# Kernel optimization log

Hardware: AMD Instinct MI355X
Metric: run time of the kernel (lower is better)

## Reference

```python
import jax, jax.numpy as jnp
import numpy as np


def lstm_scan(x, W, U, b, hidden):
    """Keras-style LSTM. x: [B,T,D]. Returns full hidden sequence [B,T,H].
    Gate order i,f,c,o; sigmoid recurrent activation, tanh cell activation."""
    B, T, D = x.shape
    H = hidden
    # Precompute input projections for all timesteps in one big GEMM: [B,T,4H]
    xz = jnp.einsum('btd,dk->btk', x, W) + b
    xz = jnp.transpose(xz, (1, 0, 2))  # [T,B,4H] for scan

    def step(carry, xz_t):
        h, c = carry
        z = xz_t + h @ U  # [B,4H]
        i = jax.nn.sigmoid(z[:, 0*H:1*H])
        f = jax.nn.sigmoid(z[:, 1*H:2*H])
        g = jnp.tanh(z[:, 2*H:3*H])
        o = jax.nn.sigmoid(z[:, 3*H:4*H])
        c_new = f * c + i * g
        h_new = o * jnp.tanh(c_new)
        return (h_new, c_new), h_new

    h0 = jnp.zeros((B, H), dtype=x.dtype)
    c0 = jnp.zeros((B, H), dtype=x.dtype)
    _, hs = jax.lax.scan(step, (h0, c0), xz)  # hs: [T,B,H]
    return jnp.transpose(hs, (1, 0, 2))  # [B,T,H]


def setup_inputs() -> dict:
    key = jax.random.key(0)
    ks = jax.random.split(key, 9)
    B, T, D = 512, 512, 300
    H1, H2, C = 128, 32, 14
    s = lambda fan: 1.0 / np.sqrt(fan)
    return {
        'x':  jax.random.normal(ks[0], (B, T, D), dtype=jnp.float32),
        'W1': jax.random.normal(ks[1], (D, 4 * H1), dtype=jnp.float32) * s(D),
        'U1': jax.random.normal(ks[2], (H1, 4 * H1), dtype=jnp.float32) * s(H1),
        'b1': jnp.zeros((4 * H1,), dtype=jnp.float32),
        'W2': jax.random.normal(ks[3], (H1, 4 * H2), dtype=jnp.float32) * s(H1),
        'U2': jax.random.normal(ks[4], (H2, 4 * H2), dtype=jnp.float32) * s(H2),
        'b2': jnp.zeros((4 * H2,), dtype=jnp.float32),
        'Wd': jax.random.normal(ks[5], (H2, C), dtype=jnp.float32) * s(H2),
        'bd': jnp.zeros((C,), dtype=jnp.float32),
    }


def reference(x, W1, U1, b1, W2, U2, b2, Wd, bd):
    h1 = lstm_scan(x, W1, U1, b1, 128)      # [B,T,128] (return_sequences=True)
    h2 = lstm_scan(h1, W2, U2, b2, 32)      # [B,T,32]
    h2_last = h2[:, -1, :]                  # return_sequences=False -> last step
    return jax.nn.softmax(h2_last @ Wd + bd, axis=-1)  # [B,14]
```

## Files before the change

kernel.cpp:

```cpp
#include <hip/hip_runtime.h>
#include <math.h>

#define TC 128
#define NC 4
#define BATCH 512
#define T_TOTAL 512
#define D_IN 300
#define KP1 320
#define H1 128
#define G1 512
#define H2 32
#define NCLS 14

typedef unsigned short u16;
typedef __attribute__((ext_vector_type(8))) _Float16 f16x8;
typedef __attribute__((ext_vector_type(4))) float f32x4;

__device__ __forceinline__ float fexp2(float x) { return __builtin_amdgcn_exp2f(x); }
__device__ __forceinline__ float frcp(float x)  { return __builtin_amdgcn_rcpf(x); }
__device__ __forceinline__ float sig_f(float x) { return frcp(1.0f + fexp2(-1.44269504f * x)); }
__device__ __forceinline__ float th_f(float x)  { return 1.0f - 2.0f * frcp(1.0f + fexp2(2.88539008f * x)); }

__device__ __forceinline__ void lds_barrier() {
    asm volatile("s_waitcnt lgkmcnt(0)" ::: "memory");
    __builtin_amdgcn_s_barrier();
}

__global__ void prep_weights(const float* __restrict__ U1, _Float16* __restrict__ U1p,
                             const float* __restrict__ U2, _Float16* __restrict__ U2p,
                             const float* __restrict__ W1, _Float16* __restrict__ W1T,
                             const float* __restrict__ W2, _Float16* __restrict__ W2T,
                             const float* __restrict__ b1, float* __restrict__ b1p,
                             const float* __restrict__ b2, float* __restrict__ b2p)
{
    int idx = blockIdx.x * 256 + threadIdx.x;
    if (idx < 512 * 128) {
        int p = idx >> 7, k = idx & 127;
        int orig = ((p >> 4) & 3) * 128 + ((p >> 6) << 4) + (p & 15);
        U1p[p * 128 + k] = (_Float16)U1[k * 512 + orig];
    }
    if (idx < 512 * 320) {
        int p = idx / 320, k = idx % 320;
        int orig = ((p >> 4) & 3) * 128 + ((p >> 6) << 4) + (p & 15);
        W1T[p * 320 + k] = (_Float16)((k < D_IN) ? W1[k * 512 + orig] : 0.f);
    }
    if (idx < 128 * 128) {
        int p = idx >> 7, k = idx & 127;
        int orig = ((p >> 4) & 3) * 32 + ((p >> 6) << 4) + (p & 15);
        W2T[p * 128 + k] = (_Float16)W2[k * 128 + orig];
    }
    if (idx < 128 * 32) {
        int p = idx >> 5, k = idx & 31;
        int orig = ((p >> 4) & 3) * 32 + ((p >> 6) << 4) + (p & 15);
        U2p[p * 32 + k] = (_Float16)U2[k * 128 + orig];
    }
    if (idx < 512) {
        int orig = ((idx >> 4) & 3) * 128 + ((idx >> 6) << 4) + (idx & 15);
        b1p[idx] = b1[orig];
    }
    if (idx < 128) {
        int orig = ((idx >> 4) & 3) * 32 + ((idx >> 6) << 4) + (idx & 15);
        b2p[idx] = b2[orig];
    }
}

__device__ __forceinline__ void xsplit_item(const float* __restrict__ x,
                                            _Float16* __restrict__ xh,
                                            int chunk, long i)
{
    int rr = (int)(i / 40), s = (int)(i % 40);
    int b = rr >> 7, tt = rr & 127;
    long m = (long)b * T_TOTAL + (long)chunk * TC + tt;
    int k0 = s * 8;
    const float* xr = x + m * D_IN + k0;
    float4 v0 = {0.f, 0.f, 0.f, 0.f}, v1 = {0.f, 0.f, 0.f, 0.f};
    if (s < 37) {
        v0 = *(const float4*)(xr);
        v1 = *(const float4*)(xr + 4);
    } else if (s == 37) {
        v0 = *(const float4*)(xr);
    }
    f16x8 o;
    o[0] = (_Float16)v0.x; o[1] = (_Float16)v0.y;
    o[2] = (_Float16)v0.z; o[3] = (_Float16)v0.w;
    o[4] = (_Float16)v1.x; o[5] = (_Float16)v1.y;
    o[6] = (_Float16)v1.z; o[7] = (_Float16)v1.w;
    *(f16x8*)(xh + m * KP1 + k0) = o;
}

__global__ void xsplit_chunk(const float* __restrict__ x, _Float16* __restrict__ xh, int chunk)
{
    long gid = (long)blockIdx.x * 256 + threadIdx.x;
    if (gid >= 65536L * 40) return;
    xsplit_item(x, xh, chunk, gid);
}

__device__ __forceinline__ void xsplit_role(const float* __restrict__ x,
                                            _Float16* __restrict__ xh,
                                            int chunk, int cwid, int ncw)
{
    const int tid = threadIdx.x;
    for (long i = (long)cwid * 512 + tid; i < 65536L * 40; i += (long)ncw * 512)
        xsplit_item(x, xh, chunk, i);
}

template<int NK, int NT, bool XMAP>
__device__ __forceinline__ void gemm_mblock(
    const _Float16* __restrict__ A, const _Float16* __restrict__ B,
    const float* __restrict__ bias, float* __restrict__ C,
    int m0, int chunk)
{
    const int Nc = NT * 128;
    const int tid = threadIdx.x;
    const int l = tid & 63, w = tid >> 6;
    const int wm = w >> 2, wn = w & 3;
    const int lr = l & 15, q = l >> 4;
    const int koff = q * 8;
    const int LDA = NK * 32;

    const _Float16* ap[4];
#pragma unroll
    for (int fi = 0; fi < 4; fi++) {
        int m = m0 + wm * 64 + fi * 16 + lr;
        long row = XMAP ? ((long)(m >> 7) * T_TOTAL + (long)chunk * TC + (m & (TC - 1)))
                        : (long)m;
        ap[fi] = A + row * LDA + koff;
    }
    const _Float16* bp[NT * 2];
    float bv[NT * 2];
#pragma unroll
    for (int fj = 0; fj < NT * 2; fj++) {
        int col = (fj >> 1) * 128 + wn * 32 + (fj & 1) * 16 + lr;
        bp[fj] = B + (long)col * LDA + koff;
        bv[fj] = bias[col];
    }

    f32x4 acc[4][NT * 2];
#pragma unroll
    for (int fi = 0; fi < 4; fi++)
#pragma unroll
        for (int fj = 0; fj < NT * 2; fj++)
            acc[fi][fj] = (f32x4){bv[fj], bv[fj], bv[fj], bv[fj]};

    f16x8 acur[4], anxt[4];
#pragma unroll
    for (int fi = 0; fi < 4; fi++)
        acur[fi] = *(const f16x8*)(ap[fi]);

#pragma unroll
    for (int ks = 0; ks < NK; ks++) {
        f16x8 bb[NT * 2];
#pragma unroll
        for (int fj = 0; fj < NT * 2; fj++)
            bb[fj] = *(const f16x8*)(bp[fj] + ks * 32);
        if (ks + 1 < NK) {
#pragma unroll
            for (int fi = 0; fi < 4; fi++)
                anxt[fi] = *(const f16x8*)(ap[fi] + (ks + 1) * 32);
        }
#pragma unroll
        for (int fi = 0; fi < 4; fi++)
#pragma unroll
            for (int fj = 0; fj < NT * 2; fj++)
                acc[fi][fj] = __builtin_amdgcn_mfma_f32_16x16x32_f16(acur[fi], bb[fj], acc[fi][fj], 0, 0, 0);
#pragma unroll
        for (int fi = 0; fi < 4; fi++)
            acur[fi] = anxt[fi];
    }

#pragma unroll
    for (int fi = 0; fi < 4; fi++) {
        int mrow = m0 + wm * 64 + fi * 16 + q * 4;
#pragma unroll
        for (int fj = 0; fj < NT * 2; fj++) {
            int col = (fj >> 1) * 128 + wn * 32 + (fj & 1) * 16 + lr;
#pragma unroll
            for (int rr = 0; rr < 4; rr++)
                C[(long)(mrow + rr) * Nc + col] = acc[fi][fj][rr];
        }
    }
}

#define L1_DECL(P) float P##0, P##1, P##2, P##3, P##4, P##5, P##6, P##7;

#define L1_LOAD(P, T)                                                             \
    P##0 = xz[xrA + (long)(T) * 512 +  0]; P##1 = xz[xrB + (long)(T) * 512 +  0]; \
    P##2 = xz[xrA + (long)(T) * 512 + 16]; P##3 = xz[xrB + (long)(T) * 512 + 16]; \
    P##4 = xz[xrA + (long)(T) * 512 + 32]; P##5 = xz[xrB + (long)(T) * 512 + 32]; \
    P##6 = xz[xrA + (long)(T) * 512 + 48]; P##7 = xz[xrB + (long)(T) * 512 + 48];

#define L1_STEP(T, PB, XC, XN)                                                    \
{                                                                                 \
    f16x8 ah0 = *(const f16x8*)&Ah[(PB) * 2048 + lr * 128 + (((q     ) ^ lr) << 3)]; \
    f16x8 ah1 = *(const f16x8*)&Ah[(PB) * 2048 + lr * 128 + (((q +  4) ^ lr) << 3)]; \
    f16x8 ah2 = *(const f16x8*)&Ah[(PB) * 2048 + lr * 128 + (((q +  8) ^ lr) << 3)]; \
    f16x8 ah3 = *(const f16x8*)&Ah[(PB) * 2048 + lr * 128 + (((q + 12) ^ lr) << 3)]; \
    if ((T) + 1 < TC) { L1_LOAD(XN, (T) + 1) }                                    \
    f32x4 a0 = (f32x4){XC##0, XC##1, 0.f, 0.f};                                   \
    f32x4 a1 = (f32x4){XC##2, XC##3, 0.f, 0.f};                                   \
    f32x4 a2 = (f32x4){XC##4, XC##5, 0.f, 0.f};                                   \
    f32x4 a3 = (f32x4){XC##6, XC##7, 0.f, 0.f};                                   \
    a0 = __builtin_amdgcn_mfma_f32_16x16x32_f16(ah0, uh00, a0, 0, 0, 0);          \
    a1 = __builtin_amdgcn_mfma_f32_16x16x32_f16(ah0, uh10, a1, 0, 0, 0);          \
    a2 = __builtin_amdgcn_mfma_f32_16x16x32_f16(ah0, uh20, a2, 0, 0, 0);          \
    a3 = __builtin_amdgcn_mfma_f32_16x16x32_f16(ah0, uh30, a3, 0, 0, 0);          \
    a0 = __builtin_amdgcn_mfma_f32_16x16x32_f16(ah1, uh01, a0, 0, 0, 0);          \
    a1 = __builtin_amdgcn_mfma_f32_16x16x32_f16(ah1, uh11, a1, 0, 0, 0);          \
    a2 = __builtin_amdgcn_mfma_f32_16x16x32_f16(ah1, uh21, a2, 0, 0, 0);          \
    a3 = __builtin_amdgcn_mfma_f32_16x16x32_f16(ah1, uh31, a3, 0, 0, 0);          \
    a0 = __builtin_amdgcn_mfma_f32_16x16x32_f16(ah2, uh02, a0, 0, 0, 0);          \
    a1 = __builtin_amdgcn_mfma_f32_16x16x32_f16(ah2, uh12, a1, 0, 0, 0);          \
    a2 = __builtin_amdgcn_mfma_f32_16x16x32_f16(ah2, uh22, a2, 0, 0, 0);          \
    a3 = __builtin_amdgcn_mfma_f32_16x16x32_f16(ah2, uh32, a3, 0, 0, 0);          \
    a0 = __builtin_amdgcn_mfma_f32_16x16x32_f16(ah3, uh03, a0, 0, 0, 0);          \
    a1 = __builtin_amdgcn_mfma_f32_16x16x32_f16(ah3, uh13, a1, 0, 0, 0);          \
    a2 = __builtin_amdgcn_mfma_f32_16x16x32_f16(ah3, uh23, a2, 0, 0, 0);          \
    a3 = __builtin_amdgcn_mfma_f32_16x16x32_f16(ah3, uh33, a3, 0, 0, 0);          \
    {                                                                             \
        float iv = sig_f(a0[0]), fv = sig_f(a1[0]), gv = th_f(a2[0]), ov = sig_f(a3[0]); \
        cstA = fv * cstA + iv * gv;                                               \
        float hv = ov * th_f(cstA);                                               \
        _Float16 hh = (_Float16)hv;                                               \
        Ah[((PB) ^ 1) * 2048 + pA * 128 + idxA] = hh;                             \
        h1f[((long)(b0 + rA) * TC + (T)) * 128 + cn] = hh;                        \
        if ((T) == TC - 1) {                                                      \
            s1h[(long)(b0 + rA) * 128 + cn] = hv;                                 \
            s1c[(long)(b0 + rA) * 128 + cn] = cstA;                               \
        }                                                                         \
    }                                                                             \
    {                                                                             \
        float iv = sig_f(a0[1]), fv = sig_f(a1[1]), gv = th_f(a2[1]), ov = sig_f(a3[1]); \
        cstB = fv * cstB + iv * gv;                                               \
        float hv = ov * th_f(cstB);                                               \
        _Float16 hh = (_Float16)hv;                                               \
        Ah[((PB) ^ 1) * 2048 + pB * 128 + idxB] = hh;                             \
        h1f[((long)(b0 + rB) * TC + (T)) * 128 + cn] = hh;                        \
        if ((T) == TC - 1) {                                                      \
            s1h[(long)(b0 + rB) * 128 + cn] = hv;                                 \
            s1c[(long)(b0 + rB) * 128 + cn] = cstB;                               \
        }                                                                         \
    }                                                                             \
    lds_barrier();                                                                \
}

static __device__ __forceinline__ void lstm1_role(
    const float* __restrict__ xz, const _Float16* __restrict__ U1p,
    _Float16* __restrict__ h1f, float* __restrict__ s1h, float* __restrict__ s1c,
    int first, char* smc)
{
    const int tid = threadIdx.x;
    const int l = tid & 63, w = tid >> 6;
    const int lr = l & 15, q = l >> 4;
    const int koff = q * 8;
    const int cn = w * 16 + lr;
    const int b0 = blockIdx.x * 8;
    const int p0 = w * 64 + lr;
    const int rA = 2 * q, rB = 2 * q + 1;
    const int pA = 4 * q, pB = 4 * q + 1;
    const int idxA = (((cn >> 3) ^ pA) << 3) + (cn & 7);
    const int idxB = (((cn >> 3) ^ pB) << 3) + (cn & 7);

    _Float16* Ah = (_Float16*)smc;

    const long xrA = ((long)(b0 + rA) * TC) * 512 + p0;
    const long xrB = ((long)(b0 + rB) * TC) * 512 + p0;

    const _Float16* ub = U1p + (long)(w * 64 + lr) * 128 + koff;
    f16x8 uh00 = *(const f16x8*)(ub +    0 * 128 +  0);
    f16x8 uh01 = *(const f16x8*)(ub +    0 * 128 + 32);
    f16x8 uh02 = *(const f16x8*)(ub +    0 * 128 + 64);
    f16x8 uh03 = *(const f16x8*)(ub +    0 * 128 + 96);
    f16x8 uh10 = *(const f16x8*)(ub +   16 * 128 +  0);
    f16x8 uh11 = *(const f16x8*)(ub +   16 * 128 + 32);
    f16x8 uh12 = *(const f16x8*)(ub +   16 * 128 + 64);
    f16x8 uh13 = *(const f16x8*)(ub +   16 * 128 + 96);
    f16x8 uh20 = *(const f16x8*)(ub +   32 * 128 +  0);
    f16x8 uh21 = *(const f16x8*)(ub +   32 * 128 + 32);
    f16x8 uh22 = *(const f16x8*)(ub +   32 * 128 + 64);
    f16x8 uh23 = *(const f16x8*)(ub +   32 * 128 + 96);
    f16x8 uh30 = *(const f16x8*)(ub +   48 * 128 +  0);
    f16x8 uh31 = *(const f16x8*)(ub +   48 * 128 + 32);
    f16x8 uh32 = *(const f16x8*)(ub +   48 * 128 + 64);
    f16x8 uh33 = *(const f16x8*)(ub +   48 * 128 + 96);

    float hA = 0.f, hB = 0.f, cstA = 0.f, cstB = 0.f;
    if (!first) {
        hA = s1h[(long)(b0 + rA) * 128 + cn];
        cstA = s1c[(long)(b0 + rA) * 128 + cn];
        hB = s1h[(long)(b0 + rB) * 128 + cn];
        cstB = s1c[(long)(b0 + rB) * 128 + cn];
    }
    Ah[pA * 128 + idxA] = (_Float16)hA;
    Ah[pB * 128 + idxB] = (_Float16)hB;
    {
        int p2 = 4 * q + 2, p3 = 4 * q + 3;
        int idx2 = (((cn >> 3) ^ p2) << 3) + (cn & 7);
        int idx3 = (((cn >> 3) ^ p3) << 3) + (cn & 7);
        Ah[p2 * 128 + idx2] = (_Float16)0.f;
        Ah[p3 * 128 + idx3] = (_Float16)0.f;
        Ah[2048 + p2 * 128 + idx2] = (_Float16)0.f;
        Ah[2048 + p3 * 128 + idx3] = (_Float16)0.f;
    }
    lds_barrier();

    L1_DECL(xa) L1_DECL(xb)
    L1_LOAD(xa, 0)

    for (int t = 0; t < TC; t += 2) {
        L1_STEP(t,     0, xa, xb)
        L1_STEP(t + 1, 1, xb, xa)
    }
}

#define L2_DECL(P) float P##00, P##01, P##02, P##03, P##10, P##11, P##12, P##13, \
                         P##20, P##21, P##22, P##23, P##30, P##31, P##32, P##33;

#define L2_LOAD(P, T)                                                             \
    P##00 = xz2[yr0 + (long)(T) * 128 +  0]; P##01 = xz2[yr1 + (long)(T) * 128 +  0]; \
    P##02 = xz2[yr2 + (long)(T) * 128 +  0]; P##03 = xz2[yr3 + (long)(T) * 128 +  0]; \
    P##10 = xz2[yr0 + (long)(T) * 128 + 16]; P##11 = xz2[yr1 + (long)(T) * 128 + 16]; \
    P##12 = xz2[yr2 + (long)(T) * 128 + 16]; P##13 = xz2[yr3 + (long)(T) * 128 + 16]; \
    P##20 = xz2[yr0 + (long)(T) * 128 + 32]; P##21 = xz2[yr1 + (long)(T) * 128 + 32]; \
    P##22 = xz2[yr2 + (long)(T) * 128 + 32]; P##23 = xz2[yr3 + (long)(T) * 128 + 32]; \
    P##30 = xz2[yr0 + (long)(T) * 128 + 48]; P##31 = xz2[yr1 + (long)(T) * 128 + 48]; \
    P##32 = xz2[yr2 + (long)(T) * 128 + 48]; P##33 = xz2[yr3 + (long)(T) * 128 + 48];

#define L2_STEP(T, PB, XC, XN)                                                    \
{                                                                                 \
    if (act) {                                                                    \
        f16x8 ah = *(const f16x8*)&Ah[(PB) * 640 + lr * 40 + koff];               \
        if ((T) + 1 < TC) { L2_LOAD(XN, (T) + 1) }                                \
        f32x4 a0 = (f32x4){XC##00, XC##01, XC##02, XC##03};                       \
        f32x4 a1 = (f32x4){XC##10, XC##11, XC##12, XC##13};                       \
        f32x4 a2 = (f32x4){XC##20, XC##21, XC##22, XC##23};                       \
        f32x4 a3 = (f32x4){XC##30, XC##31, XC##32, XC##33};                       \
        a0 = __builtin_amdgcn_mfma_f32_16x16x32_f16(ah, uh0, a0, 0, 0, 0);        \
        a1 = __builtin_amdgcn_mfma_f32_16x16x32_f16(ah, uh1, a1, 0, 0, 0);        \
        a2 = __builtin_amdgcn_mfma_f32_16x16x32_f16(ah, uh2, a2, 0, 0, 0);        \
        a3 = __builtin_amdgcn_mfma_f32_16x16x32_f16(ah, uh3, a3, 0, 0, 0);        \
        _Pragma("unroll")                                                         \
        for (int r = 0; r < 4; r++) {                                             \
            float iv = sig_f(a0[r]);                                              \
            float fv = sig_f(a1[r]);                                              \
            float gv = th_f(a2[r]);                                               \
            float ov = sig_f(a3[r]);                                              \
            float cc = (r == 0) ? cst0 : (r == 1) ? cst1 : (r == 2) ? cst2 : cst3;\
            cc = fv * cc + iv * gv;                                               \
            float hv = ov * th_f(cc);                                             \
            if (r == 0) cst0 = cc; else if (r == 1) cst1 = cc;                    \
            else if (r == 2) cst2 = cc; else cst3 = cc;                           \
            int rw = (q << 2) + r;                                                \
            Ah[((PB) ^ 1) * 640 + rw * 40 + cn] = (_Float16)hv;                   \
            if ((T) == TC - 1) {                                                  \
                s2h[(long)(b0 + rw) * 32 + cn] = hv;                              \
                s2c[(long)(b0 + rw) * 32 + cn] = cc;                              \
            }                                                                     \
        }                                                                         \
    }                                                                             \
    lds_barrier();                                                                \
}

static __device__ __forceinline__ void lstm2_role(
    const float* __restrict__ xz2, const _Float16* __restrict__ U2p,
    float* __restrict__ s2h, float* __restrict__ s2c, int first, char* smc)
{
    const int tid = threadIdx.x;
    const int b0 = (blockIdx.x - 64) * 16;
    const bool act = tid < 128;
    const int l = tid & 63, w = (tid >> 6) & 1;
    const int lr = l & 15, q = l >> 4;
    const int koff = q * 8;
    const int cn = w * 16 + lr;
    const int p0 = w * 64 + lr;
    const int bq = b0 + q * 4;

    const long yr0 = ((long)(bq + 0) * TC) * 128 + p0;
    const long yr1 = ((long)(bq + 1) * TC) * 128 + p0;
    const long yr2 = ((long)(bq + 2) * TC) * 128 + p0;
    const long yr3 = ((long)(bq + 3) * TC) * 128 + p0;

    _Float16* Ah = (_Float16*)smc;

    f16x8 uh0 = {}, uh1 = {}, uh2 = {}, uh3 = {};
    float cst0 = 0.f, cst1 = 0.f, cst2 = 0.f, cst3 = 0.f;
    L2_DECL(xa) L2_DECL(xb)

    if (act) {
        const _Float16* ub = U2p + (long)(w * 64 + lr) * 32 + koff;
        uh0 = *(const f16x8*)(ub +  0 * 32);
        uh1 = *(const f16x8*)(ub + 16 * 32);
        uh2 = *(const f16x8*)(ub + 32 * 32);
        uh3 = *(const f16x8*)(ub + 48 * 32);
#pragma unroll
        for (int r = 0; r < 4; r++) {
            int rw = q * 4 + r;
            float h = 0.f, c = 0.f;
            if (!first) {
                h = s2h[(long)(b0 + rw) * 32 + cn];
                c = s2c[(long)(b0 + rw) * 32 + cn];
            }
            if (r == 0) cst0 = c; else if (r == 1) cst1 = c;
            else if (r == 2) cst2 = c; else cst3 = c;
            Ah[rw * 40 + cn] = (_Float16)h;
        }
        L2_LOAD(xa, 0)
    }
    lds_barrier();

    for (int t = 0; t < TC; t += 2) {
        L2_STEP(t,     0, xa, xb)
        L2_STEP(t + 1, 1, xb, xa)
    }
}

__global__ void
__attribute__((amdgpu_flat_work_group_size(512, 512)))
__attribute__((amdgpu_waves_per_eu(2, 2)))
mega(
    const float* __restrict__ x, _Float16* __restrict__ xh,
    const _Float16* __restrict__ W1T, const float* __restrict__ b1p,
    const _Float16* __restrict__ W2T, const float* __restrict__ b2p,
    const _Float16* __restrict__ U1p, const _Float16* __restrict__ U2p,
    float* xz1_0, float* xz1_1, float* xz2_0, float* xz2_1,
    _Float16* h1f_0, _Float16* h1f_1,
    float* s1h, float* s1c, float* s2h, float* s2c,
    int cA, int cB, int g1, int g2, int xs)
{
    __shared__ __align__(16) char sm[8192];
    int bid = blockIdx.x;

    if (cA >= 0 && bid < 64) {
        const float* xz = (cA & 1) ? xz1_1 : xz1_0;
        _Float16* hf = (cA & 1) ? h1f_1 : h1f_0;
        lstm1_role(xz, U1p, hf, s1h, s1c, cA == 0, sm);
        return;
    }
    if (cB >= 0 && bid >= 64 && bid < 96) {
        const float* xz2 = (cB & 1) ? xz2_1 : xz2_0;
        lstm2_role(xz2, U2p, s2h, s2c, cB == 0, sm);
        return;
    }
    int cwid = bid, ncw = 256;
    if (cA >= 0) { ncw -= 64; cwid -= 64; }
    if (cB >= 0) { ncw -= 32; if (bid >= 96) cwid -= 32; }
    if (xs >= 0) xsplit_role(x, xh, xs, cwid, ncw);
    int ng1 = (g1 >= 0) ? (BATCH * TC / 128) : 0;
    int ng2 = (g2 >= 0) ? (BATCH * TC / 128) : 0;
    float* xz1o = (g1 >= 0 && (g1 & 1)) ? xz1_1 : xz1_0;
    float* xz2o = (g2 >= 0 && (g2 & 1)) ? xz2_1 : xz2_0;
    const _Float16* hf = (g2 >= 0 && (g2 & 1)) ? h1f_1 : h1f_0;
    for (int it = cwid; it < ng1 + ng2; it += ncw) {
        if (it < ng1)
            gemm_mblock<10, 4, true>(xh, W1T, b1p, xz1o, it * 128, g1);
        else
            gemm_mblock<4, 1, false>(hf, W2T, b2p, xz2o, (it - ng1) * 128, 0);
    }
}

__global__ __launch_bounds__(256)
void head_kernel(const float* __restrict__ h2, const float* __restrict__ Wd,
                 const float* __restrict__ bd, float* __restrict__ out)
{
    int b = blockIdx.x * 256 + threadIdx.x;
    float h[H2];
#pragma unroll
    for (int k = 0; k < H2; k += 4)
        *(float4*)&h[k] = *(const float4*)&h2[b * H2 + k];

    float lg[NCLS];
#pragma unroll
    for (int c = 0; c < NCLS; c++) lg[c] = bd[c];
#pragma unroll
    for (int k = 0; k < H2; k++) {
        float hv = h[k];
#pragma unroll
        for (int c = 0; c < NCLS; c++)
            lg[c] += hv * Wd[k * NCLS + c];
    }
    float m = lg[0];
#pragma unroll
    for (int c = 1; c < NCLS; c++) m = fmaxf(m, lg[c]);
    float s = 0.f;
#pragma unroll
    for (int c = 0; c < NCLS; c++) { lg[c] = __expf(lg[c] - m); s += lg[c]; }
    float inv = __fdividef(1.0f, s);
#pragma unroll
    for (int c = 0; c < NCLS; c++) out[b * NCLS + c] = lg[c] * inv;
}

extern "C" void kernel_launch(void* const* d_in, const int* in_sizes, int n_in,
                              void* d_out, int out_size, void* d_ws, size_t ws_size,
                              hipStream_t stream)
{
    const float* x  = (const float*)d_in[0];
    const float* W1 = (const float*)d_in[1];
    const float* U1 = (const float*)d_in[2];
    const float* b1 = (const float*)d_in[3];
    const float* W2 = (const float*)d_in[4];
    const float* U2 = (const float*)d_in[5];
    const float* b2 = (const float*)d_in[6];
    const float* Wd = (const float*)d_in[7];
    const float* bd = (const float*)d_in[8];
    float* out = (float*)d_out;

    char* ws = (char*)d_ws;
    float* xz1[2]    = {(float*)(ws + 0L),         (float*)(ws + 134217728L)};
    _Float16* xh     = (_Float16*)(ws + 268435456L);
    _Float16* h1f[2] = {(_Float16*)(ws + 436207616L), (_Float16*)(ws + 452984832L)};
    float* xz2[2]    = {(float*)(ws + 469762048L), (float*)(ws + 503316480L)};
    float* s1h       = (float*)(ws + 536870912L);
    float* s1c       = (float*)(ws + 537133056L);
    float* s2h       = (float*)(ws + 537395200L);
    float* s2c       = (float*)(ws + 537460736L);
    _Float16* U1p    = (_Float16*)(ws + 537526272L);
    _Float16* U2p    = (_Float16*)(ws + 537657344L);
    _Float16* W1T    = (_Float16*)(ws + 537665536L);
    _Float16* W2T    = (_Float16*)(ws + 537993216L);
    float* b1p       = (float*)(ws + 538025984L);
    float* b2p       = (float*)(ws + 538028032L);

    prep_weights<<<640, 256, 0, stream>>>(U1, U1p, U2, U2p, W1, W1T, W2, W2T,
                                          b1, b1p, b2, b2p);
    xsplit_chunk<<<10240, 256, 0, stream>>>(x, xh, 0);

#define MEGA(cA_, cB_, g1_, g2_, xs_) \
    mega<<<256, 512, 0, stream>>>(x, xh, W1T, b1p, W2T, b2p, U1p, U2p, \
        xz1[0], xz1[1], xz2[0], xz2[1], h1f[0], h1f[1], \
        s1h, s1c, s2h, s2c, cA_, cB_, g1_, g2_, xs_)

    MEGA(-1, -1, 0, -1, 1);
    MEGA(0, -1, 1, -1, 2);
    MEGA(1, -1, 2, 0, 3);
    MEGA(2, 0, 3, 1, -1);
    MEGA(3, 1, -1, 2, -1);
    MEGA(-1, 2, -1, 3, -1);
    MEGA(-1, 3, -1, -1, -1);
#undef MEGA

    head_kernel<<<2, 256, 0, stream>>>(s2h, Wd, bd, out);
}
```

Before: 917.1 us.

## Split LSTM1 recurrence across 128 blocks with 4 batch rows each

The layer-1 recurrent role now handles 4 batch rows per workgroup instead of 8, so each lane processes one row and 128 blocks share the recurrence. To make room, the persistent mega kernel launches 512 blocks and raises waves_per_eu to 4, and the GEMM/xsplit worker indexing is recomputed to skip the LSTM blocks. The aim is to shorten the serial per-step critical path and raise occupancy. In exchange, half of each MFMA's accumulator rows do no useful work, the U1 fragments are loaded by twice as many blocks, and the tighter register budget may cause spills.

```diff
diff --git a/kernel.cpp b/kernel.cpp
--- a/kernel.cpp
+++ b/kernel.cpp
@@ -181,13 +181,13 @@
     }
 }
 
-#define L1_DECL(P) float P##0, P##1, P##2, P##3, P##4, P##5, P##6, P##7;
+#define L1_DECL(P) float P##0, P##1, P##2, P##3;
 
 #define L1_LOAD(P, T)                                                             \
-    P##0 = xz[xrA + (long)(T) * 512 +  0]; P##1 = xz[xrB + (long)(T) * 512 +  0]; \
-    P##2 = xz[xrA + (long)(T) * 512 + 16]; P##3 = xz[xrB + (long)(T) * 512 + 16]; \
-    P##4 = xz[xrA + (long)(T) * 512 + 32]; P##5 = xz[xrB + (long)(T) * 512 + 32]; \
-    P##6 = xz[xrA + (long)(T) * 512 + 48]; P##7 = xz[xrB + (long)(T) * 512 + 48];
+    P##0 = xz[xr + (long)(T) * 512 +  0];                                         \
+    P##1 = xz[xr + (long)(T) * 512 + 16];                                         \
+    P##2 = xz[xr + (long)(T) * 512 + 32];                                         \
+    P##3 = xz[xr + (long)(T) * 512 + 48];
 
 #define L1_STEP(T, PB, XC, XN)                                                    \
 {                                                                                 \
@@ -196,10 +196,10 @@
     f16x8 ah2 = *(const f16x8*)&Ah[(PB) * 2048 + lr * 128 + (((q +  8) ^ lr) << 3)]; \
     f16x8 ah3 = *(const f16x8*)&Ah[(PB) * 2048 + lr * 128 + (((q + 12) ^ lr) << 3)]; \
     if ((T) + 1 < TC) { L1_LOAD(XN, (T) + 1) }                                    \
-    f32x4 a0 = (f32x4){XC##0, XC##1, 0.f, 0.f};                                   \
-    f32x4 a1 = (f32x4){XC##2, XC##3, 0.f, 0.f};                                   \
-    f32x4 a2 = (f32x4){XC##4, XC##5, 0.f, 0.f};                                   \
-    f32x4 a3 = (f32x4){XC##6, XC##7, 0.f, 0.f};                                   \
+    f32x4 a0 = (f32x4){XC##0, 0.f, 0.f, 0.f};                                     \
+    f32x4 a1 = (f32x4){XC##1, 0.f, 0.f, 0.f};                                     \
+    f32x4 a2 = (f32x4){XC##2, 0.f, 0.f, 0.f};                                     \
+    f32x4 a3 = (f32x4){XC##3, 0.f, 0.f, 0.f};                                     \
     a0 = __builtin_amdgcn_mfma_f32_16x16x32_f16(ah0, uh00, a0, 0, 0, 0);          \
     a1 = __builtin_amdgcn_mfma_f32_16x16x32_f16(ah0, uh10, a1, 0, 0, 0);          \
     a2 = __builtin_amdgcn_mfma_f32_16x16x32_f16(ah0, uh20, a2, 0, 0, 0);          \
@@ -218,26 +218,14 @@
     a3 = __builtin_amdgcn_mfma_f32_16x16x32_f16(ah3, uh33, a3, 0, 0, 0);          \
     {                                                                             \
         float iv = sig_f(a0[0]), fv = sig_f(a1[0]), gv = th_f(a2[0]), ov = sig_f(a3[0]); \
-        cstA = fv * cstA + iv * gv;                                               \
-        float hv = ov * th_f(cstA);                                               \
+        cst = fv * cst + iv * gv;                                                 \
+        float hv = ov * th_f(cst);                                                \
         _Float16 hh = (_Float16)hv;                                               \
-        Ah[((PB) ^ 1) * 2048 + pA * 128 + idxA] = hh;                             \
-        h1f[((long)(b0 + rA) * TC + (T)) * 128 + cn] = hh;                        \
+        Ah[((PB) ^ 1) * 2048 + pq * 128 + idxq] = hh;                             \
+        h1f[((long)(b0 + q) * TC + (T)) * 128 + cn] = hh;                         \
         if ((T) == TC - 1) {                                                      \
-            s1h[(long)(b0 + rA) * 128 + cn] = hv;                                 \
-            s1c[(long)(b0 + rA) * 128 + cn] = cstA;                               \
-        }                                                                         \
-    }                                                                             \
-    {                                                                             \
-        float iv = sig_f(a0[1]), fv = sig_f(a1[1]), gv = th_f(a2[1]), ov = sig_f(a3[1]); \
-        cstB = fv * cstB + iv * gv;                                               \
-        float hv = ov * th_f(cstB);                                               \
-        _Float16 hh = (_Float16)hv;                                               \
-        Ah[((PB) ^ 1) * 2048 + pB * 128 + idxB] = hh;                             \
-        h1f[((long)(b0 + rB) * TC + (T)) * 128 + cn] = hh;                        \
-        if ((T) == TC - 1) {                                                      \
-            s1h[(long)(b0 + rB) * 128 + cn] = hv;                                 \
-            s1c[(long)(b0 + rB) * 128 + cn] = cstB;                               \
+            s1h[(long)(b0 + q) * 128 + cn] = hv;                                  \
+            s1c[(long)(b0 + q) * 128 + cn] = cst;                                 \
         }                                                                         \
     }                                                                             \
     lds_barrier();                                                                \
@@ -246,24 +234,21 @@
 static __device__ __forceinline__ void lstm1_role(
     const float* __restrict__ xz, const _Float16* __restrict__ U1p,
     _Float16* __restrict__ h1f, float* __restrict__ s1h, float* __restrict__ s1c,
-    int first, char* smc)
+    int first, char* smc, int g)
 {
     const int tid = threadIdx.x;
     const int l = tid & 63, w = tid >> 6;
     const int lr = l & 15, q = l >> 4;
     const int koff = q * 8;
     const int cn = w * 16 + lr;
-    const int b0 = blockIdx.x * 8;
+    const int b0 = g * 4;
     const int p0 = w * 64 + lr;
-    const int rA = 2 * q, rB = 2 * q + 1;
-    const int pA = 4 * q, pB = 4 * q + 1;
-    const int idxA = (((cn >> 3) ^ pA) << 3) + (cn & 7);
-    const int idxB = (((cn >> 3) ^ pB) << 3) + (cn & 7);
+    const int pq = 4 * q;
+    const int idxq = (((cn >> 3) ^ pq) << 3) + (cn & 7);
 
     _Float16* Ah = (_Float16*)smc;
 
-    const long xrA = ((long)(b0 + rA) * TC) * 512 + p0;
-    const long xrB = ((long)(b0 + rB) * TC) * 512 + p0;
+    const long xr = ((long)(b0 + q) * TC) * 512 + p0;
 
     const _Float16* ub = U1p + (long)(w * 64 + lr) * 128 + koff;
     f16x8 uh00 = *(const f16x8*)(ub +    0 * 128 +  0);
@@ -283,23 +268,18 @@
     f16x8 uh32 = *(const f16x8*)(ub +   48 * 128 + 64);
     f16x8 uh33 = *(const f16x8*)(ub +   48 * 128 + 96);
 
-    float hA = 0.f, hB = 0.f, cstA = 0.f, cstB = 0.f;
+    float h = 0.f, cst = 0.f;
     if (!first) {
-        hA = s1h[(long)(b0 + rA) * 128 + cn];
-        cstA = s1c[(long)(b0 + rA) * 128 + cn];
-        hB = s1h[(long)(b0 + rB) * 128 + cn];
-        cstB = s1c[(long)(b0 + rB) * 128 + cn];
-    }
-    Ah[pA * 128 + idxA] = (_Float16)hA;
-    Ah[pB * 128 + idxB] = (_Float16)hB;
-    {
-        int p2 = 4 * q + 2, p3 = 4 * q + 3;
-        int idx2 = (((cn >> 3) ^ p2) << 3) + (cn & 7);
-        int idx3 = (((cn >> 3) ^ p3) << 3) + (cn & 7);
-        Ah[p2 * 128 + idx2] = (_Float16)0.f;
-        Ah[p3 * 128 + idx3] = (_Float16)0.f;
-        Ah[2048 + p2 * 128 + idx2] = (_Float16)0.f;
-        Ah[2048 + p3 * 128 + idx3] = (_Float16)0.f;
+        h = s1h[(long)(b0 + q) * 128 + cn];
+        cst = s1c[(long)(b0 + q) * 128 + cn];
+    }
+    Ah[pq * 128 + idxq] = (_Float16)h;
+#pragma unroll
+    for (int j = 1; j < 4; j++) {
+        int p = 4 * q + j;
+        int idx = (((cn >> 3) ^ p) << 3) + (cn & 7);
+        Ah[p * 128 + idx] = (_Float16)0.f;
+        Ah[2048 + p * 128 + idx] = (_Float16)0.f;
     }
     lds_barrier();
 
@@ -415,7 +395,7 @@
 
 __global__ void
 __attribute__((amdgpu_flat_work_group_size(512, 512)))
-__attribute__((amdgpu_waves_per_eu(2, 2)))
+__attribute__((amdgpu_waves_per_eu(4, 4)))
 mega(
     const float* __restrict__ x, _Float16* __restrict__ xh,
     const _Float16* __restrict__ W1T, const float* __restrict__ b1p,
@@ -429,10 +409,11 @@
     __shared__ __align__(16) char sm[8192];
     int bid = blockIdx.x;
 
-    if (cA >= 0 && bid < 64) {
+    if (cA >= 0 && (bid < 64 || (bid >= 256 && bid < 320))) {
+        int g = (bid < 256) ? bid : (bid - 192);
         const float* xz = (cA & 1) ? xz1_1 : xz1_0;
         _Float16* hf = (cA & 1) ? h1f_1 : h1f_0;
-        lstm1_role(xz, U1p, hf, s1h, s1c, cA == 0, sm);
+        lstm1_role(xz, U1p, hf, s1h, s1c, cA == 0, sm, g);
         return;
     }
     if (cB >= 0 && bid >= 64 && bid < 96) {
@@ -440,9 +421,17 @@
         lstm2_role(xz2, U2p, s2h, s2c, cB == 0, sm);
         return;
     }
-    int cwid = bid, ncw = 256;
-    if (cA >= 0) { ncw -= 64; cwid -= 64; }
-    if (cB >= 0) { ncw -= 32; if (bid >= 96) cwid -= 32; }
+    int rb = 0;
+    if (cA >= 0) {
+        rb += (bid < 64) ? bid : 64;
+        int t = bid - 256; rb += (t < 0) ? 0 : ((t > 64) ? 64 : t);
+    }
+    if (cB >= 0) {
+        int t = bid - 64; rb += (t < 0) ? 0 : ((t > 32) ? 32 : t);
+    }
+    int cwid = bid - rb;
+    int ncw = 512 - ((cA >= 0) ? 128 : 0) - ((cB >= 0) ? 32 : 0);
+
     if (xs >= 0) xsplit_role(x, xh, xs, cwid, ncw);
     int ng1 = (g1 >= 0) ? (BATCH * TC / 128) : 0;
     int ng2 = (g2 >= 0) ? (BATCH * TC / 128) : 0;
@@ -524,7 +513,7 @@
     xsplit_chunk<<<10240, 256, 0, stream>>>(x, xh, 0);
 
 #define MEGA(cA_, cB_, g1_, g2_, xs_) \
-    mega<<<256, 512, 0, stream>>>(x, xh, W1T, b1p, W2T, b2p, U1p, U2p, \
+    mega<<<512, 512, 0, stream>>>(x, xh, W1T, b1p, W2T, b2p, U1p, U2p, \
         xz1[0], xz1[1], xz2[0], xz2[1], h1f[0], h1f[1], \
         s1h, s1c, s2h, s2c, cA_, cB_, g1_, g2_, xs_)
 
```

Result: slower. 2.180 ms (+137.7%).
